# Performance work log

Measured on AMD Instinct MI355X. Metric: run time of the kernel, lower is better.

The kernel has to match this reference:

```python
import jax, jax.numpy as jnp
import numpy as np

N_NODES = 50000
N_EDGES = 800000
NODE_DIM = 16
EDGE_DIM = 16
HIDDEN = 128
OUT_DIM = 4
N_BLOCKS = 3  # len(layers) - 1


def setup_inputs() -> dict:
    key = jax.random.key(0)
    ks = jax.random.split(key, 12)
    s = 0.05
    x = jax.random.normal(ks[0], (N_NODES, NODE_DIM), dtype=jnp.float32)
    edge_index = jax.random.randint(ks[1], (2, N_EDGES), 0, N_NODES, dtype=jnp.int64)
    edge_attr = jax.random.normal(ks[2], (N_EDGES, EDGE_DIM), dtype=jnp.float32)
    lift_w = jax.random.normal(ks[3], (NODE_DIM, HIDDEN), dtype=jnp.float32) * s
    lift_b = jnp.zeros((HIDDEN,), dtype=jnp.float32)
    # Stacked per-block params: root linear on x_i, message linear on [x_j || e_ij]
    root_w = jax.random.normal(ks[4], (N_BLOCKS, HIDDEN, HIDDEN), dtype=jnp.float32) * s
    root_b = jnp.zeros((N_BLOCKS, HIDDEN), dtype=jnp.float32)
    msg_w = jax.random.normal(ks[5], (N_BLOCKS, HIDDEN + EDGE_DIM, HIDDEN), dtype=jnp.float32) * s
    msg_b = jnp.zeros((N_BLOCKS, HIDDEN), dtype=jnp.float32)
    proj_w = jax.random.normal(ks[6], (HIDDEN, OUT_DIM), dtype=jnp.float32) * s
    proj_b = jnp.zeros((OUT_DIM,), dtype=jnp.float32)
    return {
        "x": x, "edge_index": edge_index, "edge_attr": edge_attr,
        "lift_w": lift_w, "lift_b": lift_b,
        "root_w": root_w, "root_b": root_b,
        "msg_w": msg_w, "msg_b": msg_b,
        "proj_w": proj_w, "proj_b": proj_b,
    }


def reference(x, edge_index, edge_attr, lift_w, lift_b, root_w, root_b, msg_w, msg_b, proj_w, proj_b):
    src = edge_index[0]  # message source j
    dst = edge_index[1]  # message target i
    n = x.shape[0]
    h = x @ lift_w + lift_b  # lift: [N, H]
    n_blocks = root_w.shape[0]
    for i in range(n_blocks):  # small fixed loop over layers
        m_in = jnp.concatenate([h[src], edge_attr], axis=-1)  # [E, H+Ed]
        msg = m_in @ msg_w[i] + msg_b[i]                       # [E, H]
        agg = jax.ops.segment_sum(msg, dst, num_segments=n)    # scatter-add [N, H]
        out = h @ root_w[i] + root_b[i] + agg + h               # conv + identity skip
        # last block runs with use_activation=False
        h = jax.nn.gelu(out) if i < n_blocks - 1 else out
    return h @ proj_w + proj_b  # projection [N, OUT_DIM]
```

## Files before the change

### kernel.cpp

```cpp
#include <hip/hip_runtime.h>

#define NN 50000
#define NE 800000
#define ND 16
#define ED 16
#define H  128
#define OD 4
#define SCAN_T 512
#define KPK 288
#define LDAK 296
#define PART 16

typedef __bf16 bf16;
typedef __attribute__((ext_vector_type(8))) __bf16 bf16x8;
typedef __attribute__((ext_vector_type(4))) float f32x4;

static __device__ __forceinline__ float bf2f(unsigned short u) {
  return __builtin_bit_cast(float, (unsigned int)u << 16);
}
static __device__ __forceinline__ unsigned short f2bfu(float f) {
  return __builtin_bit_cast(unsigned short, (bf16)f);
}
static __device__ __forceinline__ unsigned int pk2(float a, float b) {
  return (unsigned int)f2bfu(a) | ((unsigned int)f2bfu(b) << 16);
}

__global__ __launch_bounds__(256) void zero_kernel(int* __restrict__ deg,
                                                   int* __restrict__ cursor) {
  int i = blockIdx.x * 256 + threadIdx.x;
  if (i < NN) { deg[i] = 0; cursor[i] = 0; }
}

__global__ __launch_bounds__(256) void degcount_kernel(
    const int* __restrict__ ei, int* __restrict__ deg) {
  int e0 = (blockIdx.x * 256 + threadIdx.x) * 4;
  if (e0 >= NE) return;
  int4 d4 = *(const int4*)&ei[NE + e0];
  atomicAdd(&deg[d4.x], 1);
  atomicAdd(&deg[d4.y], 1);
  atomicAdd(&deg[d4.z], 1);
  atomicAdd(&deg[d4.w], 1);
}

__global__ __launch_bounds__(SCAN_T) void scan_part_kernel(
    const int* __restrict__ deg, int* __restrict__ offsets,
    int* __restrict__ tops) {
  __shared__ int s[SCAN_T];
  int t = threadIdx.x;
  int i = blockIdx.x * SCAN_T + t;
  int v = (i < NN) ? deg[i] : 0;
  s[t] = v;
  __syncthreads();
  for (int off = 1; off < SCAN_T; off <<= 1) {
    int a = (t >= off) ? s[t - off] : 0;
    __syncthreads();
    s[t] += a;
    __syncthreads();
  }
  if (i < NN) offsets[i] = s[t] - v;
  if (t == SCAN_T - 1) tops[blockIdx.x] = s[t];
}

__global__ void scan_tops_kernel(int* __restrict__ tops, int ntiles,
                                 int* __restrict__ offsets) {
  if (threadIdx.x == 0) {
    int run = 0;
    for (int b = 0; b < ntiles; ++b) { int v = tops[b]; tops[b] = run; run += v; }
    offsets[NN] = NE;
  }
}

__global__ __launch_bounds__(256) void scan_add_kernel(
    int* __restrict__ offsets, const int* __restrict__ tops) {
  int i = blockIdx.x * 256 + threadIdx.x;
  if (i < NN) offsets[i] += tops[i / SCAN_T];
}

__global__ __launch_bounds__(256) void csr_fill_kernel(
    const int* __restrict__ ei, const int* __restrict__ offsets,
    int* __restrict__ cursor, int2* __restrict__ csr) {
  int part = blockIdx.x % PART;
  int e0 = (blockIdx.x / PART) * 1024 + threadIdx.x * 4;
  if (e0 >= NE) return;
  int4 s4 = *(const int4*)&ei[e0];
  int4 d4 = *(const int4*)&ei[NE + e0];
#pragma unroll
  for (int j = 0; j < 4; ++j) {
    int dst = (&d4.x)[j];
    if ((int)(((long long)dst * PART) / NN) == part) {
      int pos = atomicAdd(&cursor[dst], 1);
      csr[offsets[dst] + pos] = make_int2((&s4.x)[j], e0 + j);
    }
  }
}

__global__ __launch_bounds__(256) void pack_w_kernel(
    const float* __restrict__ msg_w, const float* __restrict__ root_w,
    const float* __restrict__ root_b, const float* __restrict__ msg_b,
    bf16* __restrict__ Wp) {
  int idx = blockIdx.x * 256 + threadIdx.x;
  int b = idx / (128 * KPK);
  int r = idx % (128 * KPK);
  int c = r / KPK, k = r % KPK;
  float v = 0.f;
  if (k < 128)       v = root_w[((size_t)b * 128 + k) * 128 + c];
  else if (k < 256)  v = msg_w[((size_t)b * 144 + (k - 128)) * 128 + c];
  else if (k < 272)  v = msg_w[((size_t)b * 144 + 128 + (k - 256)) * 128 + c];
  else if (k == 272) v = msg_b[(size_t)b * 128 + c];
  else if (k == 273) v = root_b[(size_t)b * 128 + c];
  Wp[idx] = (bf16)v;
}

__global__ __launch_bounds__(256) void lift_kernel(
    const float* __restrict__ x, const float* __restrict__ lw,
    const float* __restrict__ lb, bf16* __restrict__ h) {
  int idx = blockIdx.x * 256 + threadIdx.x;
  int n = idx >> 7, k = idx & 127;
  float acc = lb[k];
  const float* xr = x + (size_t)n * ND;
#pragma unroll
  for (int j = 0; j < ND; ++j) acc = fmaf(xr[j], lw[j * H + k], acc);
  h[idx] = (bf16)acc;
}

__global__ __launch_bounds__(256) void gather_ea_kernel(
    const int* __restrict__ offsets, const int2* __restrict__ csr,
    const bf16* __restrict__ h, const float* __restrict__ ea,
    bf16* __restrict__ hagg, bf16* __restrict__ stat) {
  int t = threadIdx.x;
  int node = blockIdx.x * 16 + (t >> 4);
  int li = t & 15;
  int k8 = li * 8;
  int s = offsets[node], e = offsets[node + 1];
  const int* ci = (const int*)csr;
  const unsigned short* Hu = (const unsigned short*)h;

  float acc[8];
#pragma unroll
  for (int j = 0; j < 8; ++j) acc[j] = 0.f;
  float aea = 0.f;

  int p = s;
  for (; p + 4 <= e; p += 4) {
    int s0 = ci[2 * p],     e0 = ci[2 * p + 1];
    int s1 = ci[2 * p + 2], e1 = ci[2 * p + 3];
    int s2 = ci[2 * p + 4], e2 = ci[2 * p + 5];
    int s3 = ci[2 * p + 6], e3 = ci[2 * p + 7];
    uint4 v0 = *(const uint4*)&Hu[(size_t)s0 * H + k8];
    uint4 v1 = *(const uint4*)&Hu[(size_t)s1 * H + k8];
    uint4 v2 = *(const uint4*)&Hu[(size_t)s2 * H + k8];
    uint4 v3 = *(const uint4*)&Hu[(size_t)s3 * H + k8];
    float a0 = ea[(size_t)e0 * ED + li];
    float a1 = ea[(size_t)e1 * ED + li];
    float a2 = ea[(size_t)e2 * ED + li];
    float a3 = ea[(size_t)e3 * ED + li];
#pragma unroll
    for (int j = 0; j < 4; ++j) {
      unsigned int w0 = (&v0.x)[j], w1 = (&v1.x)[j], w2 = (&v2.x)[j], w3 = (&v3.x)[j];
      acc[2 * j]     += (bf2f((unsigned short)(w0 & 0xffff)) + bf2f((unsigned short)(w1 & 0xffff)))
                      + (bf2f((unsigned short)(w2 & 0xffff)) + bf2f((unsigned short)(w3 & 0xffff)));
      acc[2 * j + 1] += (bf2f((unsigned short)(w0 >> 16)) + bf2f((unsigned short)(w1 >> 16)))
                      + (bf2f((unsigned short)(w2 >> 16)) + bf2f((unsigned short)(w3 >> 16)));
    }
    aea += (a0 + a1) + (a2 + a3);
  }
  for (; p < e; ++p) {
    int s0 = ci[2 * p], e0 = ci[2 * p + 1];
    uint4 v0 = *(const uint4*)&Hu[(size_t)s0 * H + k8];
    aea += ea[(size_t)e0 * ED + li];
#pragma unroll
    for (int j = 0; j < 4; ++j) {
      unsigned int w0 = (&v0.x)[j];
      acc[2 * j]     += bf2f((unsigned short)(w0 & 0xffff));
      acc[2 * j + 1] += bf2f((unsigned short)(w0 >> 16));
    }
  }

  uint4 o;
  o.x = pk2(acc[0], acc[1]);
  o.y = pk2(acc[2], acc[3]);
  o.z = pk2(acc[4], acc[5]);
  o.w = pk2(acc[6], acc[7]);
  *(uint4*)&((unsigned short*)hagg)[(size_t)node * H + k8] = o;

  unsigned short* S = (unsigned short*)stat;
  S[(size_t)node * 32 + li] = f2bfu(aea);
  float v2 = (li == 0) ? (float)(e - s) : (li == 1 ? 1.0f : 0.0f);
  S[(size_t)node * 32 + 16 + li] = f2bfu(v2);
}

__global__ __launch_bounds__(256) void gather_h_kernel(
    const int* __restrict__ offsets, const int2* __restrict__ csr,
    const bf16* __restrict__ h, bf16* __restrict__ hagg) {
  int t = threadIdx.x;
  int node = blockIdx.x * 16 + (t >> 4);
  int li = t & 15;
  int k8 = li * 8;
  int s = offsets[node], e = offsets[node + 1];
  const int* ci = (const int*)csr;
  const unsigned short* Hu = (const unsigned short*)h;

  float acc[8];
#pragma unroll
  for (int j = 0; j < 8; ++j) acc[j] = 0.f;

  int p = s;
  for (; p + 8 <= e; p += 8) {
    uint4 v[8];
#pragma unroll
    for (int q = 0; q < 8; ++q) {
      int sq = ci[2 * (p + q)];
      v[q] = *(const uint4*)&Hu[(size_t)sq * H + k8];
    }
#pragma unroll
    for (int j = 0; j < 4; ++j) {
      float lo = 0.f, hi = 0.f;
#pragma unroll
      for (int q = 0; q < 8; ++q) {
        unsigned int w = (&v[q].x)[j];
        lo += bf2f((unsigned short)(w & 0xffff));
        hi += bf2f((unsigned short)(w >> 16));
      }
      acc[2 * j] += lo;
      acc[2 * j + 1] += hi;
    }
  }
  for (; p < e; ++p) {
    int s0 = ci[2 * p];
    uint4 v0 = *(const uint4*)&Hu[(size_t)s0 * H + k8];
#pragma unroll
    for (int j = 0; j < 4; ++j) {
      unsigned int w0 = (&v0.x)[j];
      acc[2 * j]     += bf2f((unsigned short)(w0 & 0xffff));
      acc[2 * j + 1] += bf2f((unsigned short)(w0 >> 16));
    }
  }

  uint4 o;
  o.x = pk2(acc[0], acc[1]);
  o.y = pk2(acc[2], acc[3]);
  o.z = pk2(acc[4], acc[5]);
  o.w = pk2(acc[6], acc[7]);
  *(uint4*)&((unsigned short*)hagg)[(size_t)node * H + k8] = o;
}

__global__ __launch_bounds__(256, 2) void gemm_mfma_kernel(
    bf16* __restrict__ h, const bf16* __restrict__ hagg,
    const bf16* __restrict__ stat, const bf16* __restrict__ Wp, int act) {
  __shared__ bf16 as[64 * LDAK];
  int t = threadIdx.x;
  int lane = t & 63;
  int wv = t >> 6;
  int l15 = lane & 15, g = lane >> 4;
  int c0w = wv * 32;

  bf16x8 bq[9][2];
#pragma unroll
  for (int kk = 0; kk < 9; ++kk)
#pragma unroll
    for (int ni = 0; ni < 2; ++ni)
      bq[kk][ni] = *(const bf16x8*)(Wp + (size_t)(c0w + ni * 16 + l15) * KPK + kk * 32 + g * 8);

  int m0 = blockIdx.x * 64;
#pragma unroll
  for (int i = 0; i < 9; ++i) {
    int idx = i * 256 + t;
    int r = idx / 36, seg = idx % 36;
    int node = m0 + r;
    float4 v = make_float4(0.f, 0.f, 0.f, 0.f);
    if (node < NN) {
      const bf16* src;
      if (seg < 16)      src = h    + (size_t)node * H + seg * 8;
      else if (seg < 32) src = hagg + (size_t)node * H + (seg - 16) * 8;
      else               src = stat + (size_t)node * 32 + (seg - 32) * 8;
      v = *(const float4*)src;
    }
    *(float4*)(as + r * LDAK + seg * 8) = v;
  }
  __syncthreads();

  f32x4 acc[4][2];
#pragma unroll
  for (int mi = 0; mi < 4; ++mi)
#pragma unroll
    for (int ni = 0; ni < 2; ++ni)
      acc[mi][ni] = (f32x4){0.f, 0.f, 0.f, 0.f};

#pragma unroll
  for (int kk = 0; kk < 9; ++kk) {
    bf16x8 af[4];
#pragma unroll
    for (int mi = 0; mi < 4; ++mi)
      af[mi] = *(const bf16x8*)(as + (mi * 16 + l15) * LDAK + kk * 32 + g * 8);
#pragma unroll
    for (int mi = 0; mi < 4; ++mi)
#pragma unroll
      for (int ni = 0; ni < 2; ++ni)
        acc[mi][ni] = __builtin_amdgcn_mfma_f32_16x16x32_bf16(
            af[mi], bq[kk][ni], acc[mi][ni], 0, 0, 0);
  }

#pragma unroll
  for (int mi = 0; mi < 4; ++mi) {
#pragma unroll
    for (int ni = 0; ni < 2; ++ni) {
#pragma unroll
      for (int i = 0; i < 4; ++i) {
        int rloc = mi * 16 + g * 4 + i;
        int row = m0 + rloc;
        int col = c0w + ni * 16 + l15;
        if (row < NN) {
          float v = acc[mi][ni][i];
          v += bf2f(__builtin_bit_cast(unsigned short, as[rloc * LDAK + col]));
          if (act) {
            float u = 0.7978845608028654f * (v + 0.044715f * v * v * v);
            v = 0.5f * v * (1.f + tanhf(u));
          }
          h[(size_t)row * H + col] = (bf16)v;
        }
      }
    }
  }
}

__global__ __launch_bounds__(256) void proj_kernel(
    const bf16* __restrict__ h, const float* __restrict__ pw,
    const float* __restrict__ pb, float* __restrict__ out) {
  int idx = blockIdx.x * 256 + threadIdx.x;
  if (idx >= NN * OD) return;
  int n = idx >> 2, o = idx & 3;
  float acc = pb[o];
  const unsigned short* hr = (const unsigned short*)(h + (size_t)n * H);
#pragma unroll
  for (int j = 0; j < H; ++j) acc = fmaf(bf2f(hr[j]), pw[j * OD + o], acc);
  out[idx] = acc;
}

extern "C" void kernel_launch(void* const* d_in, const int* in_sizes, int n_in,
                              void* d_out, int out_size, void* d_ws, size_t ws_size,
                              hipStream_t stream) {
  const float* x       = (const float*)d_in[0];
  const int*   ei      = (const int*)d_in[1];
  const float* ea      = (const float*)d_in[2];
  const float* lift_w  = (const float*)d_in[3];
  const float* lift_b  = (const float*)d_in[4];
  const float* root_w  = (const float*)d_in[5];
  const float* root_b  = (const float*)d_in[6];
  const float* msg_w   = (const float*)d_in[7];
  const float* msg_b   = (const float*)d_in[8];
  const float* proj_w  = (const float*)d_in[9];
  const float* proj_b  = (const float*)d_in[10];
  float* out = (float*)d_out;

  char* w = (char*)d_ws;
  bf16*  h      = (bf16*)w;              w += (size_t)NN * H * 2;
  bf16*  hagg   = (bf16*)w;              w += (size_t)NN * H * 2;
  bf16*  stat   = (bf16*)w;              w += (size_t)NN * 32 * 2;
  bf16*  Wp     = (bf16*)w;              w += (size_t)3 * 128 * KPK * 2;
  int2*  csr    = (int2*)w;              w += (size_t)NE * 8;
  int*   deg     = (int*)w;              w += (size_t)NN * 4;
  int*   cursor  = (int*)w;              w += (size_t)NN * 4;
  int*   offsets = (int*)w;              w += (size_t)(NN + 16) * 4;
  int*   tops    = (int*)w;

  const int ntiles = (NN + SCAN_T - 1) / SCAN_T;

  zero_kernel<<<(NN + 255) / 256, 256, 0, stream>>>(deg, cursor);
  degcount_kernel<<<(NE / 4 + 255) / 256, 256, 0, stream>>>(ei, deg);
  scan_part_kernel<<<ntiles, SCAN_T, 0, stream>>>(deg, offsets, tops);
  scan_tops_kernel<<<1, 64, 0, stream>>>(tops, ntiles, offsets);
  scan_add_kernel<<<(NN + 255) / 256, 256, 0, stream>>>(offsets, tops);
  csr_fill_kernel<<<PART * ((NE + 1023) / 1024), 256, 0, stream>>>(ei, offsets, cursor, csr);

  pack_w_kernel<<<(3 * 128 * KPK) / 256, 256, 0, stream>>>(msg_w, root_w, root_b, msg_b, Wp);
  lift_kernel<<<(NN * H) / 256, 256, 0, stream>>>(x, lift_w, lift_b, h);

  for (int b = 0; b < 3; ++b) {
    if (b == 0)
      gather_ea_kernel<<<NN / 16, 256, 0, stream>>>(offsets, csr, h, ea, hagg, stat);
    else
      gather_h_kernel<<<NN / 16, 256, 0, stream>>>(offsets, csr, h, hagg);
    gemm_mfma_kernel<<<(NN + 63) / 64, 256, 0, stream>>>(
        h, hagg, stat, Wp + (size_t)b * 128 * KPK, b < 2 ? 1 : 0);
  }

  proj_kernel<<<(NN * OD + 255) / 256, 256, 0, stream>>>(h, proj_w, proj_b, out);
}
```

Before: 304.0 us.

## Fuse projection into last GEMM, shrink gather unroll, halve CSR fill partitions

```diff
diff --git a/kernel.cpp b/kernel.cpp
--- a/kernel.cpp
+++ b/kernel.cpp
@@ -9,7 +9,6 @@
 #define SCAN_T 512
 #define KPK 288
 #define LDAK 296
-#define PART 16
 
 typedef __bf16 bf16;
 typedef __attribute__((ext_vector_type(8))) __bf16 bf16x8;
@@ -79,15 +78,15 @@
 __global__ __launch_bounds__(256) void csr_fill_kernel(
     const int* __restrict__ ei, const int* __restrict__ offsets,
     int* __restrict__ cursor, int2* __restrict__ csr) {
-  int part = blockIdx.x % PART;
-  int e0 = (blockIdx.x / PART) * 1024 + threadIdx.x * 4;
+  int part = blockIdx.x & 7;
+  int e0 = (blockIdx.x >> 3) * 1024 + threadIdx.x * 4;
   if (e0 >= NE) return;
   int4 s4 = *(const int4*)&ei[e0];
   int4 d4 = *(const int4*)&ei[NE + e0];
 #pragma unroll
   for (int j = 0; j < 4; ++j) {
     int dst = (&d4.x)[j];
-    if ((int)(((long long)dst * PART) / NN) == part) {
+    if ((int)(((long long)dst * 8) / NN) == part) {
       int pos = atomicAdd(&cursor[dst], 1);
       csr[offsets[dst] + pos] = make_int2((&s4.x)[j], e0 + j);
     }
@@ -205,24 +204,22 @@
   for (int j = 0; j < 8; ++j) acc[j] = 0.f;
 
   int p = s;
-  for (; p + 8 <= e; p += 8) {
-    uint4 v[8];
-#pragma unroll
-    for (int q = 0; q < 8; ++q) {
-      int sq = ci[2 * (p + q)];
-      v[q] = *(const uint4*)&Hu[(size_t)sq * H + k8];
-    }
+  for (; p + 4 <= e; p += 4) {
+    int s0 = ci[2 * p];
+    int s1 = ci[2 * p + 2];
+    int s2 = ci[2 * p + 4];
+    int s3 = ci[2 * p + 6];
+    uint4 v0 = *(const uint4*)&Hu[(size_t)s0 * H + k8];
+    uint4 v1 = *(const uint4*)&Hu[(size_t)s1 * H + k8];
+    uint4 v2 = *(const uint4*)&Hu[(size_t)s2 * H + k8];
+    uint4 v3 = *(const uint4*)&Hu[(size_t)s3 * H + k8];
 #pragma unroll
     for (int j = 0; j < 4; ++j) {
-      float lo = 0.f, hi = 0.f;
-#pragma unroll
-      for (int q = 0; q < 8; ++q) {
-        unsigned int w = (&v[q].x)[j];
-        lo += bf2f((unsigned short)(w & 0xffff));
-        hi += bf2f((unsigned short)(w >> 16));
-      }
-      acc[2 * j] += lo;
-      acc[2 * j + 1] += hi;
+      unsigned int w0 = (&v0.x)[j], w1 = (&v1.x)[j], w2 = (&v2.x)[j], w3 = (&v3.x)[j];
+      acc[2 * j]     += (bf2f((unsigned short)(w0 & 0xffff)) + bf2f((unsigned short)(w1 & 0xffff)))
+                      + (bf2f((unsigned short)(w2 & 0xffff)) + bf2f((unsigned short)(w3 & 0xffff)));
+      acc[2 * j + 1] += (bf2f((unsigned short)(w0 >> 16)) + bf2f((unsigned short)(w1 >> 16)))
+                      + (bf2f((unsigned short)(w2 >> 16)) + bf2f((unsigned short)(w3 >> 16)));
     }
   }
   for (; p < e; ++p) {
@@ -246,7 +243,9 @@
 
 __global__ __launch_bounds__(256, 2) void gemm_mfma_kernel(
     bf16* __restrict__ h, const bf16* __restrict__ hagg,
-    const bf16* __restrict__ stat, const bf16* __restrict__ Wp, int act) {
+    const bf16* __restrict__ stat, const bf16* __restrict__ Wp,
+    const float* __restrict__ pw, const float* __restrict__ pb,
+    float* __restrict__ out, int act) {
   __shared__ bf16 as[64 * LDAK];
   int t = threadIdx.x;
   int lane = t & 63;
@@ -300,40 +299,51 @@
             af[mi], bq[kk][ni], acc[mi][ni], 0, 0, 0);
   }
 
-#pragma unroll
-  for (int mi = 0; mi < 4; ++mi) {
-#pragma unroll
-    for (int ni = 0; ni < 2; ++ni) {
-#pragma unroll
-      for (int i = 0; i < 4; ++i) {
-        int rloc = mi * 16 + g * 4 + i;
-        int row = m0 + rloc;
-        int col = c0w + ni * 16 + l15;
-        if (row < NN) {
+  if (act) {
+#pragma unroll
+    for (int mi = 0; mi < 4; ++mi) {
+#pragma unroll
+      for (int ni = 0; ni < 2; ++ni) {
+#pragma unroll
+        for (int i = 0; i < 4; ++i) {
+          int rloc = mi * 16 + g * 4 + i;
+          int row = m0 + rloc;
+          int col = c0w + ni * 16 + l15;
+          if (row < NN) {
+            float v = acc[mi][ni][i];
+            v += bf2f(__builtin_bit_cast(unsigned short, as[rloc * LDAK + col]));
+            float u = 0.7978845608028654f * (v + 0.044715f * v * v * v);
+            v = 0.5f * v * (1.f + tanhf(u));
+            h[(size_t)row * H + col] = (bf16)v;
+          }
+        }
+      }
+    }
+  } else {
+    __syncthreads();
+#pragma unroll
+    for (int mi = 0; mi < 4; ++mi) {
+#pragma unroll
+      for (int ni = 0; ni < 2; ++ni) {
+#pragma unroll
+        for (int i = 0; i < 4; ++i) {
+          int rloc = mi * 16 + g * 4 + i;
+          int col = c0w + ni * 16 + l15;
           float v = acc[mi][ni][i];
           v += bf2f(__builtin_bit_cast(unsigned short, as[rloc * LDAK + col]));
-          if (act) {
-            float u = 0.7978845608028654f * (v + 0.044715f * v * v * v);
-            v = 0.5f * v * (1.f + tanhf(u));
-          }
-          h[(size_t)row * H + col] = (bf16)v;
+          as[rloc * LDAK + col] = (bf16)v;
         }
       }
     }
-  }
-}
-
-__global__ __launch_bounds__(256) void proj_kernel(
-    const bf16* __restrict__ h, const float* __restrict__ pw,
-    const float* __restrict__ pb, float* __restrict__ out) {
-  int idx = blockIdx.x * 256 + threadIdx.x;
-  if (idx >= NN * OD) return;
-  int n = idx >> 2, o = idx & 3;
-  float acc = pb[o];
-  const unsigned short* hr = (const unsigned short*)(h + (size_t)n * H);
-#pragma unroll
-  for (int j = 0; j < H; ++j) acc = fmaf(bf2f(hr[j]), pw[j * OD + o], acc);
-  out[idx] = acc;
+    __syncthreads();
+    int row = t >> 2, o = t & 3;
+    float accp = pb[o];
+    const unsigned short* hr = (const unsigned short*)(as + row * LDAK);
+#pragma unroll
+    for (int j = 0; j < H; ++j)
+      accp = fmaf(bf2f(hr[j]), pw[j * OD + o], accp);
+    if (m0 + row < NN) out[(size_t)(m0 + row) * OD + o] = accp;
+  }
 }
 
 extern "C" void kernel_launch(void* const* d_in, const int* in_sizes, int n_in,
@@ -370,7 +380,7 @@
   scan_part_kernel<<<ntiles, SCAN_T, 0, stream>>>(deg, offsets, tops);
   scan_tops_kernel<<<1, 64, 0, stream>>>(tops, ntiles, offsets);
   scan_add_kernel<<<(NN + 255) / 256, 256, 0, stream>>>(offsets, tops);
-  csr_fill_kernel<<<PART * ((NE + 1023) / 1024), 256, 0, stream>>>(ei, offsets, cursor, csr);
+  csr_fill_kernel<<<8 * ((NE + 1023) / 1024), 256, 0, stream>>>(ei, offsets, cursor, csr);
 
   pack_w_kernel<<<(3 * 128 * KPK) / 256, 256, 0, stream>>>(msg_w, root_w, root_b, msg_b, Wp);
   lift_kernel<<<(NN * H) / 256, 256, 0, stream>>>(x, lift_w, lift_b, h);
@@ -381,8 +391,7 @@
     else
       gather_h_kernel<<<NN / 16, 256, 0, stream>>>(offsets, csr, h, hagg);
     gemm_mfma_kernel<<<(NN + 63) / 64, 256, 0, stream>>>(
-        h, hagg, stat, Wp + (size_t)b * 128 * KPK, b < 2 ? 1 : 0);
-  }
-
-  proj_kernel<<<(NN * OD + 255) / 256, 256, 0, stream>>>(h, proj_w, proj_b, out);
-}
+        h, hagg, stat, Wp + (size_t)b * 128 * KPK,
+        proj_w, proj_b, out, b < 2 ? 1 : 0);
+  }
+}
```

New measurement: 303.3 us. About the same (-0.2%).
